# Optimization experiments

Hardware: AMD Instinct MI355X
Metric: run time of the kernel (lower is better)

## Reference

```python
import jax, jax.numpy as jnp
import numpy as np

D = 512       # d_model
H = 8         # n_heads
HD = D // H   # head_dim
LYR = 4       # number_of_layers
PMT = 20      # pmt_len
L = 2048      # decode / target length (src_len - pmt_len)
BS = 1
DOUT = 3      # d_output (3 coding classes)
DFF = 4 * D
EPS = 1e-5


def layer_norm(x, g, b):
    m = jnp.mean(x, axis=-1, keepdims=True)
    v = jnp.mean((x - m) ** 2, axis=-1, keepdims=True)
    return (x - m) * jax.lax.rsqrt(v + EPS) * g + b


def rope(x):
    # x: (b, h, s, hd); half-split rotary with base 10000, positions = arange(s)
    half = x.shape[-1] // 2
    pos = jnp.arange(x.shape[2], dtype=jnp.float32)
    inv_freq = 1.0 / (10000.0 ** (jnp.arange(half, dtype=jnp.float32) / half))
    ang = pos[:, None] * inv_freq[None, :]          # (s, half)
    cos = jnp.cos(ang)[None, None]                  # (1,1,s,half)
    sin = jnp.sin(ang)[None, None]
    x1, x2 = x[..., :half], x[..., half:]
    return jnp.concatenate([x1 * cos - x2 * sin, x1 * sin + x2 * cos], axis=-1)


def mha(xq, xkv, wqkv, bqkv, wo, bo, key_mask, causal):
    # xq: (b, sq, D), xkv: (b, sk, D); key_mask: (b, sk) with 1=valid
    b, sq, _ = xq.shape
    sk = xkv.shape[1]
    q = xq @ wqkv[:, :D] + bqkv[:D]
    kv = xkv @ wqkv[:, D:] + bqkv[D:]
    k, v = kv[..., :D], kv[..., D:]
    q = q.reshape(b, sq, H, HD).transpose(0, 2, 1, 3)   # (b,h,sq,hd)
    k = k.reshape(b, sk, H, HD).transpose(0, 2, 1, 3)
    v = v.reshape(b, sk, H, HD).transpose(0, 2, 1, 3)
    q = rope(q)
    k = rope(k)
    scores = jnp.einsum('bhqd,bhkd->bhqk', q, k) / jnp.sqrt(jnp.float32(HD))
    scores = scores + jnp.where(key_mask[:, None, None, :] > 0, 0.0, -1e9)
    if causal:
        cm = jnp.tril(jnp.ones((sq, sk), dtype=bool))
        scores = jnp.where(cm[None, None], scores, -1e9)
    attn = jax.nn.softmax(scores, axis=-1)
    out = jnp.einsum('bhqk,bhkd->bhqd', attn, v)
    out = out.transpose(0, 2, 1, 3).reshape(b, sq, D)
    return out @ wo + bo


def setup_inputs() -> dict:
    key = jax.random.key(0)
    ks = jax.random.split(key, 16)
    s = 0.02
    p = lambda i, shape: jax.random.normal(ks[i], shape, jnp.float32) * s
    return {
        'trg_inputs': jax.random.normal(ks[0], (BS, L, DOUT), jnp.float32),
        'src_rep': jax.random.normal(ks[1], (BS, PMT + L, D), jnp.float32),
        'src_mask': jnp.ones((BS, L), jnp.float32),
        'emb_w': p(2, (DOUT, D)), 'emb_b': jnp.zeros((D,), jnp.float32),
        'sa_wqkv': p(3, (LYR, D, 3 * D)), 'sa_bqkv': jnp.zeros((LYR, 3 * D), jnp.float32),
        'sa_wo': p(4, (LYR, D, D)), 'sa_bo': jnp.zeros((LYR, D), jnp.float32),
        'ca_wqkv': p(5, (LYR, D, 3 * D)), 'ca_bqkv': jnp.zeros((LYR, 3 * D), jnp.float32),
        'ca_wo': p(6, (LYR, D, D)), 'ca_bo': jnp.zeros((LYR, D), jnp.float32),
        'ffn_w1': p(7, (LYR, D, DFF)), 'ffn_b1': jnp.zeros((LYR, DFF), jnp.float32),
        'ffn_w2': p(8, (LYR, DFF, D)), 'ffn_b2': jnp.zeros((LYR, D), jnp.float32),
        'ln_g': jnp.ones((LYR, 3, D), jnp.float32), 'ln_b': jnp.zeros((LYR, 3, D), jnp.float32),
        'lnf_g': jnp.ones((D,), jnp.float32), 'lnf_b': jnp.zeros((D,), jnp.float32),
        'gen_w': p(9, (D, DOUT)), 'gen_b': jnp.zeros((DOUT,), jnp.float32),
    }


def reference(trg_inputs, src_rep, src_mask, emb_w, emb_b, sa_wqkv, sa_bqkv, sa_wo, sa_bo,
              ca_wqkv, ca_bqkv, ca_wo, ca_bo, ffn_w1, ffn_b1, ffn_w2, ffn_b2,
              ln_g, ln_b, lnf_g, lnf_b, gen_w, gen_b):
    srb = src_rep[:, PMT:, :]                       # (bs, L, D)
    x = trg_inputs @ emb_w + emb_b                  # (bs, L, D)
    trg_mask = src_mask                             # parallel mode: trg_mask = src_mask
    for li in range(LYR):
        h = layer_norm(x, ln_g[li, 0], ln_b[li, 0])
        x = x + mha(h, h, sa_wqkv[li], sa_bqkv[li], sa_wo[li], sa_bo[li], trg_mask, causal=True)
        h = layer_norm(x, ln_g[li, 1], ln_b[li, 1])
        x = x + mha(h, srb, ca_wqkv[li], ca_bqkv[li], ca_wo[li], ca_bo[li], src_mask, causal=False)
        h = layer_norm(x, ln_g[li, 2], ln_b[li, 2])
        x = x + (jax.nn.relu(h @ ffn_w1[li] + ffn_b1[li]) @ ffn_w2[li] + ffn_b2[li])
    x = layer_norm(x, lnf_g, lnf_b)
    return x @ gen_w + gen_b                        # logits (bs, L, 3)
```

## Files before the change

### kernel.cpp

```cpp
#include <hip/hip_runtime.h>
#include <hip/hip_bf16.h>

#define SEQ 2048
#define DM 512
#define NHEAD 8
#define HDIM 64
#define DFFN 2048
#define PMTN 20

typedef __bf16 bf16x8 __attribute__((ext_vector_type(8)));
typedef float f32x4 __attribute__((ext_vector_type(4)));
typedef unsigned short u16x8 __attribute__((ext_vector_type(8)));

__device__ __forceinline__ float wave_sum(float v) {
#pragma unroll
  for (int off = 32; off; off >>= 1) v += __shfl_xor(v, off);
  return v;
}

__device__ __forceinline__ unsigned short f2b(float x) {
  __hip_bfloat16 h = __float2bfloat16(x);
  return *(unsigned short*)&h;
}

__device__ __forceinline__ void gll16(const __hip_bfloat16* g, __hip_bfloat16* l) {
  __builtin_amdgcn_global_load_lds(
      (const __attribute__((address_space(1))) unsigned int*)(g),
      (__attribute__((address_space(3))) unsigned int*)(l), 16, 0, 0);
}

__global__ __launch_bounds__(256) void embed_kernel(
    const float* __restrict__ trg, const float* __restrict__ w,
    const float* __restrict__ b, float* __restrict__ X) {
  int idx = blockIdx.x * 256 + threadIdx.x;
  int r = idx >> 9, c = idx & 511;
  float t0 = trg[r * 3 + 0], t1 = trg[r * 3 + 1], t2 = trg[r * 3 + 2];
  X[idx] = t0 * w[c] + t1 * w[512 + c] + t2 * w[1024 + c] + b[c];
}

__global__ __launch_bounds__(256) void cast_bf16_kernel(
    const float* __restrict__ in, __hip_bfloat16* __restrict__ out) {
  int i = blockIdx.x * 256 + threadIdx.x;
  out[i] = __float2bfloat16(in[i]);
}

__global__ __launch_bounds__(256) void rope_table_kernel(float2* __restrict__ rt) {
  int idx = blockIdx.x * 256 + threadIdx.x;
  int row = idx >> 5, i = idx & 31;
  float inv = __expf(-(float)i * (9.210340371976184f / 32.f));
  float sn, cs;
  sincosf((float)row * inv, &sn, &cs);
  rt[idx] = make_float2(cs, sn);
}

__global__ __launch_bounds__(256) void mbias_kernel(
    const float* __restrict__ mask, float* __restrict__ mb,
    int* __restrict__ mtflag) {
  int i = blockIdx.x * 256 + threadIdx.x;
  bool masked = !(mask[i] > 0.f);
  mb[i] = masked ? -8.0e9f : 0.f;
  unsigned long long any = __ballot(masked);
  if ((threadIdx.x & 63) == 0) mtflag[i >> 6] = (any != 0ull) ? 1 : 0;
}

__global__ __launch_bounds__(256) void ln_bf16_kernel(
    const float* __restrict__ x, const float* __restrict__ g,
    const float* __restrict__ b, __hip_bfloat16* __restrict__ o) {
  int row = blockIdx.x * 4 + (threadIdx.x >> 6);
  int lane = threadIdx.x & 63;
  const float* xr = x + (long)row * DM;
  float v[8];
  float s = 0.f;
#pragma unroll
  for (int j = 0; j < 8; j++) { v[j] = xr[lane + 64 * j]; s += v[j]; }
  s = wave_sum(s);
  float mean = s * (1.f / DM);
  float q = 0.f;
#pragma unroll
  for (int j = 0; j < 8; j++) { float d = v[j] - mean; q += d * d; }
  q = wave_sum(q);
  float r = rsqrtf(q * (1.f / DM) + 1e-5f);
  __hip_bfloat16* orow = o + (long)row * DM;
#pragma unroll
  for (int j = 0; j < 8; j++) {
    int c = lane + 64 * j;
    orow[c] = __float2bfloat16((v[j] - mean) * r * g[c] + b[c]);
  }
}

__global__ __launch_bounds__(256) void ln_gen_kernel(
    const float* __restrict__ x, const float* __restrict__ g,
    const float* __restrict__ b, const float* __restrict__ gw,
    const float* __restrict__ gb, float* __restrict__ out) {
  int row = blockIdx.x * 4 + (threadIdx.x >> 6);
  int lane = threadIdx.x & 63;
  const float* xr = x + (long)row * DM;
  float v[8];
  float s = 0.f;
#pragma unroll
  for (int j = 0; j < 8; j++) { v[j] = xr[lane + 64 * j]; s += v[j]; }
  s = wave_sum(s);
  float mean = s * (1.f / DM);
  float q = 0.f;
#pragma unroll
  for (int j = 0; j < 8; j++) { float d = v[j] - mean; q += d * d; }
  q = wave_sum(q);
  float r = rsqrtf(q * (1.f / DM) + 1e-5f);
  float a0 = 0.f, a1 = 0.f, a2 = 0.f;
#pragma unroll
  for (int j = 0; j < 8; j++) {
    int c = lane + 64 * j;
    float nv = (v[j] - mean) * r * g[c] + b[c];
    a0 = fmaf(nv, gw[c * 3 + 0], a0);
    a1 = fmaf(nv, gw[c * 3 + 1], a1);
    a2 = fmaf(nv, gw[c * 3 + 2], a2);
  }
  a0 = wave_sum(a0);
  a1 = wave_sum(a1);
  a2 = wave_sum(a2);
  if (lane == 0) {
    out[row * 3 + 0] = a0 + gb[0];
    out[row * 3 + 1] = a1 + gb[1];
    out[row * 3 + 2] = a2 + gb[2];
  }
}

__global__ __launch_bounds__(256) void transpose_layer_kernel(
    const float* __restrict__ wqkv, const float* __restrict__ wo,
    const float* __restrict__ cwqkv, const float* __restrict__ cwo,
    const float* __restrict__ w1, const float* __restrict__ w2,
    __hip_bfloat16* __restrict__ Wt) {
  int b = blockIdx.x;
  const float* W;
  __hip_bfloat16* O;
  int Kd, Nd;
  if (b < 192)      { W = wqkv;  O = Wt + 0;       Kd = 512;  Nd = 1536; }
  else if (b < 256) { W = wo;    O = Wt + 786432;  Kd = 512;  Nd = 512;  b -= 192; }
  else if (b < 448) { W = cwqkv; O = Wt + 1048576; Kd = 512;  Nd = 1536; b -= 256; }
  else if (b < 512) { W = cwo;   O = Wt + 1835008; Kd = 512;  Nd = 512;  b -= 448; }
  else if (b < 768) { W = w1;    O = Wt + 2097152; Kd = 512;  Nd = 2048; b -= 512; }
  else              { W = w2;    O = Wt + 3145728; Kd = 2048; Nd = 512;  b -= 768; }
  int tn = Nd >> 6;
  int k0 = (b / tn) * 64, n0 = (b % tn) * 64;
  __shared__ float T[64][65];
  int t = threadIdx.x;
  int rr = t >> 4, c4 = (t & 15) * 4;
#pragma unroll
  for (int p = 0; p < 4; p++) {
    int row = rr + p * 16;
    float4 v = *(const float4*)(W + (long)(k0 + row) * Nd + n0 + c4);
    T[row][c4 + 0] = v.x; T[row][c4 + 1] = v.y;
    T[row][c4 + 2] = v.z; T[row][c4 + 3] = v.w;
  }
  __syncthreads();
#pragma unroll
  for (int p = 0; p < 4; p++) {
    int row = rr + p * 16;
    ushort4 pk;
    pk.x = f2b(T[c4 + 0][row]); pk.y = f2b(T[c4 + 1][row]);
    pk.z = f2b(T[c4 + 2][row]); pk.w = f2b(T[c4 + 3][row]);
    *(ushort4*)(O + (long)(n0 + row) * Kd + k0 + c4) = pk;
  }
}

__global__ __launch_bounds__(256) void gemm_bf16_64(
    const __hip_bfloat16* __restrict__ A, int lda,
    const __hip_bfloat16* __restrict__ A2,
    const __hip_bfloat16* __restrict__ Bt, int ldb,
    const float* __restrict__ bias,
    const float* __restrict__ residual,
    float* __restrict__ Cf, __hip_bfloat16* __restrict__ Cb, int ldc,
    int K, int relu, int mode, const float2* __restrict__ rt,
    __hip_bfloat16* __restrict__ Qp, __hip_bfloat16* __restrict__ Kp,
    __hip_bfloat16* __restrict__ Vtp) {
  __shared__ __attribute__((aligned(16))) __hip_bfloat16 As[2][4096];
  __shared__ __attribute__((aligned(16))) __hip_bfloat16 Bs[2][4096];
  const int t = threadIdx.x;
  const int bx = blockIdx.x;
  const int nrow = bx * 64, m0 = blockIdx.y * 64;
  const int ptype = (mode == 0) ? 3 : (nrow < 512 ? 0 : (nrow < 1024 ? 1 : 2));
  const int head = (nrow >> 6) & 7;
  const __hip_bfloat16* Ause = (mode == 2 && bx >= 8) ? A2 : A;

  const int w = t >> 6, lane = t & 63;
  const int wr = w >> 1, wc = w & 1;
  const int fr = lane & 15, fk = lane >> 4;
  const int r0 = t & 63, c0 = t >> 6;
  const __hip_bfloat16* Arow = Ause + (long)(m0 + r0) * lda;
  const __hip_bfloat16* Brow = Bt + (long)(nrow + r0) * ldb;

  uint4 ra0 = *(const uint4*)(Arow + c0 * 8);
  uint4 ra1 = *(const uint4*)(Arow + (c0 + 4) * 8);
  uint4 rb0 = *(const uint4*)(Brow + c0 * 8);
  uint4 rb1 = *(const uint4*)(Brow + (c0 + 4) * 8);
  *(uint4*)(&As[0][(c0 * 64 + r0) * 8]) = ra0;
  *(uint4*)(&As[0][((c0 + 4) * 64 + r0) * 8]) = ra1;
  *(uint4*)(&Bs[0][(c0 * 64 + r0) * 8]) = rb0;
  *(uint4*)(&Bs[0][((c0 + 4) * 64 + r0) * 8]) = rb1;
  __syncthreads();

  f32x4 acc[2][2] = {};
  const int NK = K >> 6;
  for (int ks = 0; ks < NK; ++ks) {
    const int cur = ks & 1;
    if (ks + 1 < NK) {
      const int ko = (ks + 1) << 6;
      ra0 = *(const uint4*)(Arow + ko + c0 * 8);
      ra1 = *(const uint4*)(Arow + ko + (c0 + 4) * 8);
      rb0 = *(const uint4*)(Brow + ko + c0 * 8);
      rb1 = *(const uint4*)(Brow + ko + (c0 + 4) * 8);
    }
#pragma unroll
    for (int kk = 0; kk < 2; ++kk) {
      const int kc = kk * 4 + fk;
      bf16x8 a0 = *(const bf16x8*)(&As[cur][(kc * 64 + wr * 32 + fr) * 8]);
      bf16x8 a1 = *(const bf16x8*)(&As[cur][(kc * 64 + wr * 32 + 16 + fr) * 8]);
      bf16x8 b0 = *(const bf16x8*)(&Bs[cur][(kc * 64 + wc * 32 + fr) * 8]);
      bf16x8 b1 = *(const bf16x8*)(&Bs[cur][(kc * 64 + wc * 32 + 16 + fr) * 8]);
      acc[0][0] = __builtin_amdgcn_mfma_f32_16x16x32_bf16(a0, b0, acc[0][0], 0, 0, 0);
      acc[0][1] = __builtin_amdgcn_mfma_f32_16x16x32_bf16(a0, b1, acc[0][1], 0, 0, 0);
      acc[1][0] = __builtin_amdgcn_mfma_f32_16x16x32_bf16(a1, b0, acc[1][0], 0, 0, 0);
      acc[1][1] = __builtin_amdgcn_mfma_f32_16x16x32_bf16(a1, b1, acc[1][1], 0, 0, 0);
    }
    if (ks + 1 < NK) {
      const int nxt = cur ^ 1;
      *(uint4*)(&As[nxt][(c0 * 64 + r0) * 8]) = ra0;
      *(uint4*)(&As[nxt][((c0 + 4) * 64 + r0) * 8]) = ra1;
      *(uint4*)(&Bs[nxt][(c0 * 64 + r0) * 8]) = rb0;
      *(uint4*)(&Bs[nxt][((c0 + 4) * 64 + r0) * 8]) = rb1;
    }
    __syncthreads();
  }

  if (ptype == 3) {
#pragma unroll
    for (int m = 0; m < 2; ++m)
#pragma unroll
      for (int n = 0; n < 2; ++n)
#pragma unroll
        for (int j = 0; j < 4; ++j) {
          int r = m0 + wr * 32 + m * 16 + fk * 4 + j;
          int c = nrow + wc * 32 + n * 16 + fr;
          float v = acc[m][n][j] + bias[c];
          if (relu) v = fmaxf(v, 0.f);
          if (residual) v += residual[(long)r * ldc + c];
          if (Cf) Cf[(long)r * ldc + c] = v;
          if (Cb) Cb[(long)r * ldc + c] = __float2bfloat16(v);
        }
    return;
  }

  float* Lt = (float*)As;
#pragma unroll
  for (int m = 0; m < 2; ++m)
#pragma unroll
    for (int n = 0; n < 2; ++n)
#pragma unroll
      for (int j = 0; j < 4; ++j) {
        int rl = wr * 32 + m * 16 + fk * 4 + j;
        int cl = wc * 32 + n * 16 + fr;
        Lt[rl * 64 + (cl ^ (rl & 31))] = acc[m][n][j] + bias[nrow + cl];
      }
  __syncthreads();

  if (ptype == 2) {
    const int d = t >> 2, sc = (t & 3) * 16;
    u16x8 o0, o1;
#pragma unroll
    for (int s = 0; s < 8; s++) {
      o0[s] = f2b(Lt[(sc + s) * 64 + (d ^ ((sc + s) & 31))]);
      o1[s] = f2b(Lt[(sc + 8 + s) * 64 + (d ^ ((sc + 8 + s) & 31))]);
    }
    __hip_bfloat16* dst = Vtp + ((long)(head * 64 + d)) * SEQ + m0 + sc;
    *(u16x8*)dst = o0;
    *(u16x8*)(dst + 8) = o1;
  } else {
    const int r = t >> 2, i0 = (t & 3) * 8;
    const float2* rp = rt + (long)(m0 + r) * 32 + i0;
    u16x8 lo, hi;
#pragma unroll
    for (int p = 0; p < 8; p++) {
      float a = Lt[r * 64 + ((i0 + p) ^ (r & 31))];
      float b = Lt[r * 64 + ((i0 + p + 32) ^ (r & 31))];
      float2 cs = rp[p];
      lo[p] = f2b(a * cs.x - b * cs.y);
      hi[p] = f2b(a * cs.y + b * cs.x);
    }
    __hip_bfloat16* dst =
        (ptype == 0 ? Qp : Kp) + ((long)head * SEQ + m0 + r) * 64 + i0;
    *(u16x8*)dst = lo;
    *(u16x8*)(dst + 32) = hi;
  }
}

__global__ __launch_bounds__(256) void attn_part_kernel(
    const __hip_bfloat16* __restrict__ Qp, const __hip_bfloat16* __restrict__ Kp,
    const __hip_bfloat16* __restrict__ Vtp, const float* __restrict__ mbias,
    const int* __restrict__ mtflag,
    __hip_bfloat16* __restrict__ Op, float* __restrict__ Ml,
    int causal, int csz) {
  const int qt = blockIdx.x, ch = blockIdx.y, head = blockIdx.z;
  const int kv0 = ch * csz;
  if (causal && kv0 > qt * 64 + 63) return;
  const int kvlen = causal ? min(csz, qt * 64 + 64 - kv0) : csz;
  const int nt = (kvlen + 63) >> 6;

  __shared__ __attribute__((aligned(16))) __hip_bfloat16 Ks[2][4096];
  __shared__ __attribute__((aligned(16))) __hip_bfloat16 Vs[2][4096];
  __shared__ __attribute__((aligned(16))) __hip_bfloat16 Ps[4096];
  const int t = threadIdx.x, w = t >> 6, lane = t & 63;
  const int fr = lane & 15, fk = lane >> 4;
  const int qr = qt * 64 + w * 16 + fr;
  const int wq0 = qt * 64 + w * 16;
  const float SCL = 0.18033688011112042f;

  bf16x8 qa0, qa1;
  {
    const __hip_bfloat16* qp = Qp + ((long)head * SEQ + qr) * 64 + fk * 8;
    qa0 = *(const bf16x8*)qp;
    qa1 = *(const bf16x8*)(qp + 32);
  }
  const __hip_bfloat16* Kh = Kp + (long)head * SEQ * 64;
  const __hip_bfloat16* Vh = Vtp + (long)head * 64 * SEQ;
  const int skr = t & 63, skc = t >> 6;

  float m_i = -3e38f, l_i = 0.f;
  f32x4 o_[4] = {};
  const int sw2 = (fr & 7) << 4;

  {
    const __hip_bfloat16* ksrc = Kh + (long)(kv0 + skr) * 64 + skc * 8;
    gll16(ksrc, Ks[0] + t * 8);
    gll16(ksrc + 32, Ks[0] + t * 8 + 2048);
    const __hip_bfloat16* vsrc = Vh + (long)skr * SEQ + kv0 + skc * 8;
    gll16(vsrc, Vs[0] + t * 8);
    gll16(vsrc + 32, Vs[0] + t * 8 + 2048);
  }

  for (int tile = 0; tile < nt; ++tile) {
    __syncthreads();
    const int cur = tile & 1;
    if (tile + 1 < nt) {
      const int kb1 = kv0 + (tile + 1) * 64;
      const int nxt = cur ^ 1;
      const __hip_bfloat16* ksrc = Kh + (long)(kb1 + skr) * 64 + skc * 8;
      gll16(ksrc, Ks[nxt] + t * 8);
      gll16(ksrc + 32, Ks[nxt] + t * 8 + 2048);
      const __hip_bfloat16* vsrc = Vh + (long)skr * SEQ + kb1 + skc * 8;
      gll16(vsrc, Vs[nxt] + t * 8);
      gll16(vsrc + 32, Vs[nxt] + t * 8 + 2048);
    }
    const int kb = kv0 + tile * 64;
    const bool need = !causal || (kb <= wq0 + 15);
    if (need) {
      const bool diag = causal && (kb + 63 > wq0);
      const bool hasmask = mtflag[kb >> 6] != 0;

      f32x4 sacc[4];
      __builtin_amdgcn_s_setprio(1);
#pragma unroll
      for (int n = 0; n < 4; n++) {
        bf16x8 ka0 = *(const bf16x8*)(Ks[cur] + fk * 512 + (n * 16 + fr) * 8);
        bf16x8 ka1 = *(const bf16x8*)(Ks[cur] + (4 + fk) * 512 + (n * 16 + fr) * 8);
        f32x4 zz = {};
        zz = __builtin_amdgcn_mfma_f32_16x16x32_bf16(ka0, qa0, zz, 0, 0, 0);
        sacc[n] = __builtin_amdgcn_mfma_f32_16x16x32_bf16(ka1, qa1, zz, 0, 0, 0);
      }
      __builtin_amdgcn_s_setprio(0);

      float sv[4][4];
      float rm = -3e38f;
#pragma unroll
      for (int n = 0; n < 4; n++) {
        const int ka = kb + n * 16 + fk * 4;
        if (hasmask) {
          float4 mb = *(const float4*)(mbias + ka);
          sv[n][0] = sacc[n][0] + mb.x;
          sv[n][1] = sacc[n][1] + mb.y;
          sv[n][2] = sacc[n][2] + mb.z;
          sv[n][3] = sacc[n][3] + mb.w;
        } else {
          sv[n][0] = sacc[n][0]; sv[n][1] = sacc[n][1];
          sv[n][2] = sacc[n][2]; sv[n][3] = sacc[n][3];
        }
        if (diag) {
#pragma unroll
          for (int j = 0; j < 4; j++)
            if (ka + j > qr) sv[n][j] = -3e38f;
        }
#pragma unroll
        for (int j = 0; j < 4; j++) rm = fmaxf(rm, sv[n][j]);
      }
      rm = fmaxf(rm, __shfl_xor(rm, 16));
      rm = fmaxf(rm, __shfl_xor(rm, 32));
      if (!__all(rm <= m_i)) {
        float nm = fmaxf(m_i, rm);
        float f = exp2f((m_i - nm) * SCL);
        l_i *= f;
#pragma unroll
        for (int n = 0; n < 4; n++) o_[n] *= f;
        m_i = nm;
      }
      float ps = 0.f;
#pragma unroll
      for (int n = 0; n < 4; n++) {
        float p0 = exp2f((sv[n][0] - m_i) * SCL);
        float p1 = exp2f((sv[n][1] - m_i) * SCL);
        float p2 = exp2f((sv[n][2] - m_i) * SCL);
        float p3 = exp2f((sv[n][3] - m_i) * SCL);
        ps += (p0 + p1) + (p2 + p3);
        ushort4 pk4;
        pk4.x = f2b(p0); pk4.y = f2b(p1); pk4.z = f2b(p2); pk4.w = f2b(p3);
        *(ushort4*)((char*)Ps + ((w * 2048 + fr * 128 + (n * 16 + fk * 4) * 2) ^ sw2)) = pk4;
      }
      ps += __shfl_xor(ps, 16);
      ps += __shfl_xor(ps, 32);
      l_i += ps;

      __builtin_amdgcn_s_setprio(1);
#pragma unroll
      for (int s = 0; s < 2; s++) {
        bf16x8 pb = *(const bf16x8*)((char*)Ps + ((w * 2048 + fr * 128 + s * 64 + fk * 16) ^ sw2));
#pragma unroll
        for (int n = 0; n < 4; n++) {
          bf16x8 va = *(const bf16x8*)(Vs[cur] + (s * 4 + fk) * 512 + (n * 16 + fr) * 8);
          o_[n] = __builtin_amdgcn_mfma_f32_16x16x32_bf16(va, pb, o_[n], 0, 0, 0);
        }
      }
      __builtin_amdgcn_s_setprio(0);
    }
  }

  const long bid = ((long)head * 32 + qt) * gridDim.y + ch;
  __hip_bfloat16* Ob = Op + bid * 4096;
#pragma unroll
  for (int n = 0; n < 4; n++) {
    ushort4 ov;
    ov.x = f2b(o_[n][0]); ov.y = f2b(o_[n][1]);
    ov.z = f2b(o_[n][2]); ov.w = f2b(o_[n][3]);
    *(ushort4*)(Ob + (w * 16 + fr) * 64 + n * 16 + fk * 4) = ov;
  }
  if (fk == 0) {
    float2 ml = make_float2(m_i, l_i);
    *(float2*)(Ml + bid * 128 + (w * 16 + fr) * 2) = ml;
  }
}

__global__ __launch_bounds__(256) void attn_combine_kernel(
    const __hip_bfloat16* __restrict__ Op, const float* __restrict__ Ml,
    __hip_bfloat16* __restrict__ O, int ldo, int causal, int csz, int nch) {
  const int qt = blockIdx.x, head = blockIdx.y;
  const int nc = causal ? min(nch, (qt * 64 + 63) / csz + 1) : nch;
  const int t = threadIdx.x;
  const int row = t >> 2, c16 = (t & 3) * 16;
  const long bid0 = ((long)head * 32 + qt) * nch;
  const float SCL = 0.18033688011112042f;
  float M = -3e38f;
  for (int c = 0; c < nc; c++) M = fmaxf(M, Ml[(bid0 + c) * 128 + row * 2]);
  float L = 0.f;
  float acc[16] = {};
  for (int c = 0; c < nc; c++) {
    float2 ml = *(const float2*)(Ml + (bid0 + c) * 128 + row * 2);
    float wg = exp2f((ml.x - M) * SCL);
    L += wg * ml.y;
    const __hip_bfloat16* base = Op + (bid0 + c) * 4096 + row * 64 + c16;
    bf16x8 a = *(const bf16x8*)base;
    bf16x8 b = *(const bf16x8*)(base + 8);
#pragma unroll
    for (int e = 0; e < 8; e++) {
      acc[e] += wg * (float)a[e];
      acc[8 + e] += wg * (float)b[e];
    }
  }
  float invL = 1.f / fmaxf(L, 1e-20f);
  u16x8 o0, o1;
#pragma unroll
  for (int e = 0; e < 8; e++) {
    o0[e] = f2b(acc[e] * invL);
    o1[e] = f2b(acc[8 + e] * invL);
  }
  __hip_bfloat16* orow = O + (long)(qt * 64 + row) * ldo + head * 64 + c16;
  *(u16x8*)orow = o0;
  *(u16x8*)(orow + 8) = o1;
}

extern "C" void kernel_launch(void* const* d_in, const int* in_sizes, int n_in,
                              void* d_out, int out_size, void* d_ws, size_t ws_size,
                              hipStream_t stream) {
  const float* trg      = (const float*)d_in[0];
  const float* src_rep  = (const float*)d_in[1];
  const float* src_mask = (const float*)d_in[2];
  const float* emb_w    = (const float*)d_in[3];
  const float* emb_b    = (const float*)d_in[4];
  const float* sa_wqkv  = (const float*)d_in[5];
  const float* sa_bqkv  = (const float*)d_in[6];
  const float* sa_wo    = (const float*)d_in[7];
  const float* sa_bo    = (const float*)d_in[8];
  const float* ca_wqkv  = (const float*)d_in[9];
  const float* ca_bqkv  = (const float*)d_in[10];
  const float* ca_wo    = (const float*)d_in[11];
  const float* ca_bo    = (const float*)d_in[12];
  const float* ffn_w1   = (const float*)d_in[13];
  const float* ffn_b1   = (const float*)d_in[14];
  const float* ffn_w2   = (const float*)d_in[15];
  const float* ffn_b2   = (const float*)d_in[16];
  const float* ln_g     = (const float*)d_in[17];
  const float* ln_b     = (const float*)d_in[18];
  const float* lnf_g    = (const float*)d_in[19];
  const float* lnf_b    = (const float*)d_in[20];
  const float* gen_w    = (const float*)d_in[21];
  const float* gen_b    = (const float*)d_in[22];

  const float* srb = src_rep + (long)PMTN * DM;

  char* wsb = (char*)d_ws;
  float*          X    = (float*)wsb;
  __hip_bfloat16* Hb   = (__hip_bfloat16*)(wsb + (4ul << 20));
  __hip_bfloat16* MID  = (__hip_bfloat16*)(wsb + (6ul << 20));
  __hip_bfloat16* Op   = MID;
  __hip_bfloat16* AO   = (__hip_bfloat16*)(wsb + (14ul << 20));
  __hip_bfloat16* SRBb = (__hip_bfloat16*)(wsb + (16ul << 20));
  float2*         rt   = (float2*)(wsb + (18ul << 20));
  float*          mbias= (float*)(wsb + (18ul << 20) + 524288);
  int*            mtfl = (int*)(wsb + (18ul << 20) + 532480);
  float*          Ml   = (float*)(wsb + (19ul << 20));
  __hip_bfloat16* Qp   = (__hip_bfloat16*)(wsb + (20ul << 20));
  __hip_bfloat16* Kp   = (__hip_bfloat16*)(wsb + (22ul << 20));
  __hip_bfloat16* Vtp  = (__hip_bfloat16*)(wsb + (24ul << 20));
  __hip_bfloat16* Wt   = (__hip_bfloat16*)(wsb + (26ul << 20));

  const int nch = 4;
  const int csz = SEQ / nch;

  embed_kernel<<<(SEQ * DM) / 256, 256, 0, stream>>>(trg, emb_w, emb_b, X);
  cast_bf16_kernel<<<(SEQ * DM) / 256, 256, 0, stream>>>(srb, SRBb);
  rope_table_kernel<<<256, 256, 0, stream>>>(rt);
  mbias_kernel<<<8, 256, 0, stream>>>(src_mask, mbias, mtfl);

  __hip_bfloat16* wqkvT  = Wt + 0;
  __hip_bfloat16* woT    = Wt + 786432;
  __hip_bfloat16* cwqkvT = Wt + 1048576;
  __hip_bfloat16* cwoT   = Wt + 1835008;
  __hip_bfloat16* w1T    = Wt + 2097152;
  __hip_bfloat16* w2T    = Wt + 3145728;

  for (int li = 0; li < 4; li++) {
    transpose_layer_kernel<<<1024, 256, 0, stream>>>(
        sa_wqkv + (long)li * DM * 3 * DM, sa_wo + (long)li * DM * DM,
        ca_wqkv + (long)li * DM * 3 * DM, ca_wo + (long)li * DM * DM,
        ffn_w1 + (long)li * DM * DFFN, ffn_w2 + (long)li * DFFN * DM, Wt);

    const float* bqkv  = sa_bqkv + (long)li * 3 * DM;
    const float* bo    = sa_bo + (long)li * DM;
    const float* cbqkv = ca_bqkv + (long)li * 3 * DM;
    const float* cbo   = ca_bo + (long)li * DM;
    const float* b1    = ffn_b1 + (long)li * DFFN;
    const float* b2    = ffn_b2 + (long)li * DM;
    const float* g0  = ln_g + (long)(li * 3 + 0) * DM;
    const float* bb0 = ln_b + (long)(li * 3 + 0) * DM;
    const float* g1  = ln_g + (long)(li * 3 + 1) * DM;
    const float* bb1 = ln_b + (long)(li * 3 + 1) * DM;
    const float* g2  = ln_g + (long)(li * 3 + 2) * DM;
    const float* bb2 = ln_b + (long)(li * 3 + 2) * DM;

    ln_bf16_kernel<<<512, 256, 0, stream>>>(X, g0, bb0, Hb);
    gemm_bf16_64<<<dim3(24, 32), 256, 0, stream>>>(
        Hb, DM, nullptr, wqkvT, DM, bqkv, nullptr, nullptr, nullptr, DM,
        DM, 0, 1, rt, Qp, Kp, Vtp);
    attn_part_kernel<<<dim3(32, nch, 8), 256, 0, stream>>>(
        Qp, Kp, Vtp, mbias, mtfl, Op, Ml, 1, csz);
    attn_combine_kernel<<<dim3(32, 8), 256, 0, stream>>>(
        Op, Ml, AO, DM, 1, csz, nch);
    gemm_bf16_64<<<dim3(8, 32), 256, 0, stream>>>(
        AO, DM, nullptr, woT, DM, bo, X, X, nullptr, DM,
        DM, 0, 0, nullptr, nullptr, nullptr, nullptr);

    ln_bf16_kernel<<<512, 256, 0, stream>>>(X, g1, bb1, Hb);
    gemm_bf16_64<<<dim3(24, 32), 256, 0, stream>>>(
        Hb, DM, SRBb, cwqkvT, DM, cbqkv, nullptr, nullptr, nullptr, DM,
        DM, 0, 2, rt, Qp, Kp, Vtp);
    attn_part_kernel<<<dim3(32, nch, 8), 256, 0, stream>>>(
        Qp, Kp, Vtp, mbias, mtfl, Op, Ml, 0, csz);
    attn_combine_kernel<<<dim3(32, 8), 256, 0, stream>>>(
        Op, Ml, AO, DM, 0, csz, nch);
    gemm_bf16_64<<<dim3(8, 32), 256, 0, stream>>>(
        AO, DM, nullptr, cwoT, DM, cbo, X, X, nullptr, DM,
        DM, 0, 0, nullptr, nullptr, nullptr, nullptr);

    ln_bf16_kernel<<<512, 256, 0, stream>>>(X, g2, bb2, Hb);
    gemm_bf16_64<<<dim3(32, 32), 256, 0, stream>>>(
        Hb, DM, nullptr, w1T, DM, b1, nullptr, nullptr, MID, DFFN,
        DM, 1, 0, nullptr, nullptr, nullptr, nullptr);
    gemm_bf16_64<<<dim3(8, 32), 256, 0, stream>>>(
        MID, DFFN, nullptr, w2T, DFFN, b2, X, X, nullptr, DM,
        DFFN, 0, 0, nullptr, nullptr, nullptr, nullptr);
  }

  ln_gen_kernel<<<512, 256, 0, stream>>>(X, lnf_g, lnf_b, gen_w, gen_b,
                                         (float*)d_out);
}
```

Measured before the change: 758.8 us.

## Fuse attention split-combine into output projection GEMM and merge prologue kernels

Drops the separate attention combine kernel. The out-projection GEMM (mode 3) now reads the per-chunk partial outputs and max/sum statistics directly, merges them with softmax rescaling, and writes the bf16 A tile into LDS. This removes the AO round trip and one launch per attention. The four setup kernels are also merged into one prologue launch. The cost is that the combine work is repeated by each of the 8 column blocks of the GEMM, and the A-operand load path grows heavier.

Result: slower. 861.8 us (+13.6%).

```diff
diff --git a/kernel.cpp b/kernel.cpp
--- a/kernel.cpp
+++ b/kernel.cpp
@@ -29,38 +29,35 @@
       (__attribute__((address_space(3))) unsigned int*)(l), 16, 0, 0);
 }
 
-__global__ __launch_bounds__(256) void embed_kernel(
-    const float* __restrict__ trg, const float* __restrict__ w,
-    const float* __restrict__ b, float* __restrict__ X) {
-  int idx = blockIdx.x * 256 + threadIdx.x;
-  int r = idx >> 9, c = idx & 511;
-  float t0 = trg[r * 3 + 0], t1 = trg[r * 3 + 1], t2 = trg[r * 3 + 2];
-  X[idx] = t0 * w[c] + t1 * w[512 + c] + t2 * w[1024 + c] + b[c];
-}
-
-__global__ __launch_bounds__(256) void cast_bf16_kernel(
-    const float* __restrict__ in, __hip_bfloat16* __restrict__ out) {
-  int i = blockIdx.x * 256 + threadIdx.x;
-  out[i] = __float2bfloat16(in[i]);
-}
-
-__global__ __launch_bounds__(256) void rope_table_kernel(float2* __restrict__ rt) {
-  int idx = blockIdx.x * 256 + threadIdx.x;
-  int row = idx >> 5, i = idx & 31;
-  float inv = __expf(-(float)i * (9.210340371976184f / 32.f));
-  float sn, cs;
-  sincosf((float)row * inv, &sn, &cs);
-  rt[idx] = make_float2(cs, sn);
-}
-
-__global__ __launch_bounds__(256) void mbias_kernel(
-    const float* __restrict__ mask, float* __restrict__ mb,
-    int* __restrict__ mtflag) {
-  int i = blockIdx.x * 256 + threadIdx.x;
-  bool masked = !(mask[i] > 0.f);
-  mb[i] = masked ? -8.0e9f : 0.f;
-  unsigned long long any = __ballot(masked);
-  if ((threadIdx.x & 63) == 0) mtflag[i >> 6] = (any != 0ull) ? 1 : 0;
+__global__ __launch_bounds__(256) void prologue_kernel(
+    const float* __restrict__ trg, const float* __restrict__ emb_w,
+    const float* __restrict__ emb_b, float* __restrict__ X,
+    const float* __restrict__ srb, __hip_bfloat16* __restrict__ SRBb,
+    float2* __restrict__ rt, const float* __restrict__ mask,
+    float* __restrict__ mb, int* __restrict__ mtflag) {
+  const int b = blockIdx.x, t = threadIdx.x;
+  if (b < 4096) {
+    int idx = b * 256 + t;
+    int r = idx >> 9, c = idx & 511;
+    float t0 = trg[r * 3 + 0], t1 = trg[r * 3 + 1], t2 = trg[r * 3 + 2];
+    X[idx] = t0 * emb_w[c] + t1 * emb_w[512 + c] + t2 * emb_w[1024 + c] + emb_b[c];
+  } else if (b < 8192) {
+    int i = (b - 4096) * 256 + t;
+    SRBb[i] = __float2bfloat16(srb[i]);
+  } else if (b < 8448) {
+    int idx = (b - 8192) * 256 + t;
+    int row = idx >> 5, i = idx & 31;
+    float inv = __expf(-(float)i * (9.210340371976184f / 32.f));
+    float sn, cs;
+    sincosf((float)row * inv, &sn, &cs);
+    rt[idx] = make_float2(cs, sn);
+  } else {
+    int i = (b - 8448) * 256 + t;
+    bool masked = !(mask[i] > 0.f);
+    mb[i] = masked ? -8.0e9f : 0.f;
+    unsigned long long any = __ballot(masked);
+    if ((t & 63) == 0) mtflag[i >> 6] = (any != 0ull) ? 1 : 0;
+  }
 }
 
 __global__ __launch_bounds__(256) void ln_bf16_kernel(
@@ -163,6 +160,54 @@
   }
 }
 
+__device__ __forceinline__ void comb_load(
+    const __hip_bfloat16* OpP, const float* MlP, long hbase, int rin, int c0,
+    int nc3, float2* mlr, bf16x8* o0r, bf16x8* o1r) {
+#pragma unroll
+  for (int c = 0; c < 4; c++)
+    if (c < nc3) {
+      mlr[c] = *(const float2*)(MlP + (hbase + c) * 128 + rin * 2);
+      const __hip_bfloat16* ob = OpP + (hbase + c) * 4096 + (long)rin * 64;
+      o0r[c] = *(const bf16x8*)(ob + c0 * 8);
+      o1r[c] = *(const bf16x8*)(ob + (c0 + 4) * 8);
+    }
+}
+
+__device__ __forceinline__ void comb_math(
+    const float2* mlr, const bf16x8* o0r, const bf16x8* o1r, int nc3,
+    uint4& ra0, uint4& ra1) {
+  const float SCL = 0.18033688011112042f;
+  float M = -3e38f;
+#pragma unroll
+  for (int c = 0; c < 4; c++)
+    if (c < nc3) M = fmaxf(M, mlr[c].x);
+  float L = 0.f, wgi[4] = {0.f, 0.f, 0.f, 0.f};
+#pragma unroll
+  for (int c = 0; c < 4; c++)
+    if (c < nc3) {
+      wgi[c] = exp2f((mlr[c].x - M) * SCL);
+      L += wgi[c] * mlr[c].y;
+    }
+  float invL = 1.f / fmaxf(L, 1e-20f);
+#pragma unroll
+  for (int c = 0; c < 4; c++) wgi[c] *= invL;
+  float alo[8] = {}, ahi[8] = {};
+#pragma unroll
+  for (int c = 0; c < 4; c++)
+    if (c < nc3) {
+#pragma unroll
+      for (int e = 0; e < 8; e++) {
+        alo[e] = fmaf(wgi[c], (float)o0r[c][e], alo[e]);
+        ahi[e] = fmaf(wgi[c], (float)o1r[c][e], ahi[e]);
+      }
+    }
+  u16x8 plo, phi;
+#pragma unroll
+  for (int e = 0; e < 8; e++) { plo[e] = f2b(alo[e]); phi[e] = f2b(ahi[e]); }
+  ra0 = *(uint4*)&plo;
+  ra1 = *(uint4*)&phi;
+}
+
 __global__ __launch_bounds__(256) void gemm_bf16_64(
     const __hip_bfloat16* __restrict__ A, int lda,
     const __hip_bfloat16* __restrict__ A2,
@@ -172,13 +217,17 @@
     float* __restrict__ Cf, __hip_bfloat16* __restrict__ Cb, int ldc,
     int K, int relu, int mode, const float2* __restrict__ rt,
     __hip_bfloat16* __restrict__ Qp, __hip_bfloat16* __restrict__ Kp,
-    __hip_bfloat16* __restrict__ Vtp) {
+    __hip_bfloat16* __restrict__ Vtp,
+    const __hip_bfloat16* __restrict__ OpP, const float* __restrict__ MlP,
+    int cz3) {
   __shared__ __attribute__((aligned(16))) __hip_bfloat16 As[2][4096];
   __shared__ __attribute__((aligned(16))) __hip_bfloat16 Bs[2][4096];
   const int t = threadIdx.x;
   const int bx = blockIdx.x;
   const int nrow = bx * 64, m0 = blockIdx.y * 64;
-  const int ptype = (mode == 0) ? 3 : (nrow < 512 ? 0 : (nrow < 1024 ? 1 : 2));
+  const bool packE = (mode == 1 || mode == 2);
+  const int ptype = packE ? (nrow < 512 ? 0 : (nrow < 1024 ? 1 : 2)) : 3;
+  const bool combA = (mode == 3);
   const int head = (nrow >> 6) & 7;
   const __hip_bfloat16* Ause = (mode == 2 && bx >= 8) ? A2 : A;
 
@@ -189,10 +238,26 @@
   const __hip_bfloat16* Arow = Ause + (long)(m0 + r0) * lda;
   const __hip_bfloat16* Brow = Bt + (long)(nrow + r0) * ldb;
 
-  uint4 ra0 = *(const uint4*)(Arow + c0 * 8);
-  uint4 ra1 = *(const uint4*)(Arow + (c0 + 4) * 8);
-  uint4 rb0 = *(const uint4*)(Brow + c0 * 8);
-  uint4 rb1 = *(const uint4*)(Brow + (c0 + 4) * 8);
+  int qt2 = 0, rin = 0, nc3 = 0;
+  if (combA) {
+    int qrow = m0 + r0;
+    qt2 = qrow >> 6;
+    rin = qrow & 63;
+    nc3 = cz3 ? ((qt2 >> 3) + 1) : 4;
+  }
+  float2 mlr[4];
+  bf16x8 o0r[4], o1r[4];
+
+  uint4 ra0, ra1, rb0, rb1;
+  if (combA) {
+    comb_load(OpP, MlP, ((long)0 * 32 + qt2) * 4, rin, c0, nc3, mlr, o0r, o1r);
+    comb_math(mlr, o0r, o1r, nc3, ra0, ra1);
+  } else {
+    ra0 = *(const uint4*)(Arow + c0 * 8);
+    ra1 = *(const uint4*)(Arow + (c0 + 4) * 8);
+  }
+  rb0 = *(const uint4*)(Brow + c0 * 8);
+  rb1 = *(const uint4*)(Brow + (c0 + 4) * 8);
   *(uint4*)(&As[0][(c0 * 64 + r0) * 8]) = ra0;
   *(uint4*)(&As[0][((c0 + 4) * 64 + r0) * 8]) = ra1;
   *(uint4*)(&Bs[0][(c0 * 64 + r0) * 8]) = rb0;
@@ -205,8 +270,13 @@
     const int cur = ks & 1;
     if (ks + 1 < NK) {
       const int ko = (ks + 1) << 6;
-      ra0 = *(const uint4*)(Arow + ko + c0 * 8);
-      ra1 = *(const uint4*)(Arow + ko + (c0 + 4) * 8);
+      if (combA) {
+        comb_load(OpP, MlP, ((long)(ks + 1) * 32 + qt2) * 4, rin, c0, nc3,
+                  mlr, o0r, o1r);
+      } else {
+        ra0 = *(const uint4*)(Arow + ko + c0 * 8);
+        ra1 = *(const uint4*)(Arow + ko + (c0 + 4) * 8);
+      }
       rb0 = *(const uint4*)(Brow + ko + c0 * 8);
       rb1 = *(const uint4*)(Brow + ko + (c0 + 4) * 8);
     }
@@ -224,6 +294,7 @@
     }
     if (ks + 1 < NK) {
       const int nxt = cur ^ 1;
+      if (combA) comb_math(mlr, o0r, o1r, nc3, ra0, ra1);
       *(uint4*)(&As[nxt][(c0 * 64 + r0) * 8]) = ra0;
       *(uint4*)(&As[nxt][((c0 + 4) * 64 + r0) * 8]) = ra1;
       *(uint4*)(&Bs[nxt][(c0 * 64 + r0) * 8]) = rb0;
@@ -444,44 +515,6 @@
     float2 ml = make_float2(m_i, l_i);
     *(float2*)(Ml + bid * 128 + (w * 16 + fr) * 2) = ml;
   }
-}
-
-__global__ __launch_bounds__(256) void attn_combine_kernel(
-    const __hip_bfloat16* __restrict__ Op, const float* __restrict__ Ml,
-    __hip_bfloat16* __restrict__ O, int ldo, int causal, int csz, int nch) {
-  const int qt = blockIdx.x, head = blockIdx.y;
-  const int nc = causal ? min(nch, (qt * 64 + 63) / csz + 1) : nch;
-  const int t = threadIdx.x;
-  const int row = t >> 2, c16 = (t & 3) * 16;
-  const long bid0 = ((long)head * 32 + qt) * nch;
-  const float SCL = 0.18033688011112042f;
-  float M = -3e38f;
-  for (int c = 0; c < nc; c++) M = fmaxf(M, Ml[(bid0 + c) * 128 + row * 2]);
-  float L = 0.f;
-  float acc[16] = {};
-  for (int c = 0; c < nc; c++) {
-    float2 ml = *(const float2*)(Ml + (bid0 + c) * 128 + row * 2);
-    float wg = exp2f((ml.x - M) * SCL);
-    L += wg * ml.y;
-    const __hip_bfloat16* base = Op + (bid0 + c) * 4096 + row * 64 + c16;
-    bf16x8 a = *(const bf16x8*)base;
-    bf16x8 b = *(const bf16x8*)(base + 8);
-#pragma unroll
-    for (int e = 0; e < 8; e++) {
-      acc[e] += wg * (float)a[e];
-      acc[8 + e] += wg * (float)b[e];
-    }
-  }
-  float invL = 1.f / fmaxf(L, 1e-20f);
-  u16x8 o0, o1;
-#pragma unroll
-  for (int e = 0; e < 8; e++) {
-    o0[e] = f2b(acc[e] * invL);
-    o1[e] = f2b(acc[8 + e] * invL);
-  }
-  __hip_bfloat16* orow = O + (long)(qt * 64 + row) * ldo + head * 64 + c16;
-  *(u16x8*)orow = o0;
-  *(u16x8*)(orow + 8) = o1;
 }
 
 extern "C" void kernel_launch(void* const* d_in, const int* in_sizes, int n_in,
@@ -532,10 +565,8 @@
   const int nch = 4;
   const int csz = SEQ / nch;
 
-  embed_kernel<<<(SEQ * DM) / 256, 256, 0, stream>>>(trg, emb_w, emb_b, X);
-  cast_bf16_kernel<<<(SEQ * DM) / 256, 256, 0, stream>>>(srb, SRBb);
-  rope_table_kernel<<<256, 256, 0, stream>>>(rt);
-  mbias_kernel<<<8, 256, 0, stream>>>(src_mask, mbias, mtfl);
+  prologue_kernel<<<8456, 256, 0, stream>>>(trg, emb_w, emb_b, X, srb, SRBb,
+                                            rt, src_mask, mbias, mtfl);
 
   __hip_bfloat16* wqkvT  = Wt + 0;
   __hip_bfloat16* woT    = Wt + 786432;
@@ -566,34 +597,30 @@
     ln_bf16_kernel<<<512, 256, 0, stream>>>(X, g0, bb0, Hb);
     gemm_bf16_64<<<dim3(24, 32), 256, 0, stream>>>(
         Hb, DM, nullptr, wqkvT, DM, bqkv, nullptr, nullptr, nullptr, DM,
-        DM, 0, 1, rt, Qp, Kp, Vtp);
+        DM, 0, 1, rt, Qp, Kp, Vtp, nullptr, nullptr, 0);
     attn_part_kernel<<<dim3(32, nch, 8), 256, 0, stream>>>(
         Qp, Kp, Vtp, mbias, mtfl, Op, Ml, 1, csz);
-    attn_combine_kernel<<<dim3(32, 8), 256, 0, stream>>>(
-        Op, Ml, AO, DM, 1, csz, nch);
     gemm_bf16_64<<<dim3(8, 32), 256, 0, stream>>>(
         AO, DM, nullptr, woT, DM, bo, X, X, nullptr, DM,
-        DM, 0, 0, nullptr, nullptr, nullptr, nullptr);
+        DM, 0, 3, nullptr, nullptr, nullptr, nullptr, Op, Ml, 1);
 
     ln_bf16_kernel<<<512, 256, 0, stream>>>(X, g1, bb1, Hb);
     gemm_bf16_64<<<dim3(24, 32), 256, 0, stream>>>(
         Hb, DM, SRBb, cwqkvT, DM, cbqkv, nullptr, nullptr, nullptr, DM,
-        DM, 0, 2, rt, Qp, Kp, Vtp);
+        DM, 0, 2, rt, Qp, Kp, Vtp, nullptr, nullptr, 0);
     attn_part_kernel<<<dim3(32, nch, 8), 256, 0, stream>>>(
         Qp, Kp, Vtp, mbias, mtfl, Op, Ml, 0, csz);
-    attn_combine_kernel<<<dim3(32, 8), 256, 0, stream>>>(
-        Op, Ml, AO, DM, 0, csz, nch);
     gemm_bf16_64<<<dim3(8, 32), 256, 0, stream>>>(
         AO, DM, nullptr, cwoT, DM, cbo, X, X, nullptr, DM,
-        DM, 0, 0, nullptr, nullptr, nullptr, nullptr);
+        DM, 0, 3, nullptr, nullptr, nullptr, nullptr, Op, Ml, 0);
 
     ln_bf16_kernel<<<512, 256, 0, stream>>>(X, g2, bb2, Hb);
     gemm_bf16_64<<<dim3(32, 32), 256, 0, stream>>>(
         Hb, DM, nullptr, w1T, DM, b1, nullptr, nullptr, MID, DFFN,
-        DM, 1, 0, nullptr, nullptr, nullptr, nullptr);
+        DM, 1, 0, nullptr, nullptr, nullptr, nullptr, nullptr, nullptr, 0);
     gemm_bf16_64<<<dim3(8, 32), 256, 0, stream>>>(
         MID, DFFN, nullptr, w2T, DFFN, b2, X, X, nullptr, DM,
-        DFFN, 0, 0, nullptr, nullptr, nullptr, nullptr);
+        DFFN, 0, 0, nullptr, nullptr, nullptr, nullptr, nullptr, nullptr, 0);
   }
 
   ln_gen_kernel<<<512, 256, 0, stream>>>(X, lnf_g, lnf_b, gen_w, gen_b,
```
